# Performance work log

Hardware: AMD Instinct MI355X
Metric: run time of the kernel (lower is better)

## Reference

```python
import jax, jax.numpy as jnp
import numpy as np

MARGIN = 1.0

def setup_inputs() -> dict:
    key = jax.random.key(0)
    k1, k2 = jax.random.split(key)
    B, D, NUM_CLASSES = 4096, 512, 64
    inputs = jax.random.normal(k1, (B, D), dtype=jnp.float32)
    labels = jax.random.randint(k2, (B,), 0, NUM_CLASSES, dtype=jnp.int64)
    return {"inputs": inputs, "labels": labels}

def reference(inputs, labels):
    # Full pairwise squared L2 distances via the ||a-b||^2 = ||a||^2 + ||b||^2 - 2 a.b expansion
    sq = jnp.sum(inputs * inputs, axis=1)                      # [B]
    d2 = sq[:, None] + sq[None, :] - 2.0 * (inputs @ inputs.T)  # [B, B]
    d2 = jnp.maximum(d2, 0.0)
    # Safe sqrt: zero (self) distances get exactly 0 without NaN-producing sqrt(0) grads
    nz = d2 > 1e-12
    dist = jnp.where(nz, jnp.sqrt(jnp.where(nz, d2, 1.0)), 0.0)  # [B, B]

    mask = labels[:, None] == labels[None, :]                   # [B, B] same-class mask (includes self)
    mask_f = mask.astype(dist.dtype)

    # Per-anchor: mean distance to positives (self included, contributing 0, as in the torch loop)
    ap_mean = jnp.sum(dist * mask_f, axis=1) / jnp.sum(mask_f, axis=1)  # [B]
    # Per-anchor: min distance to negatives
    an_min = jnp.min(jnp.where(mask, jnp.inf, dist), axis=1)            # [B]

    tmp = ap_mean - an_min + MARGIN                             # [B]
    # `if tmp > 0: loss += tmp` over the batch == sum of relu(tmp)
    return jnp.sum(jnp.maximum(tmp, 0.0))
```

## Files before the change

kernel.cpp:

```cpp
#include <hip/hip_runtime.h>
#include <hip/hip_bf16.h>

typedef unsigned short u16;
typedef unsigned int u32;
typedef __attribute__((ext_vector_type(8))) short short8;
typedef __attribute__((ext_vector_type(8))) u16 ushort8;
typedef __attribute__((ext_vector_type(4))) float f32x4;

#define B_SZ 4096
#define D_SZ 512
#define NCLS 64
#define NT   32
#define NBLK (NT * (NT + 1) / 2)


__device__ __forceinline__ u16 f2bf(float x) {
    union { float f; u32 u; } a; a.f = x;
    u32 r = a.u + 0x7fffu + ((a.u >> 16) & 1u);
    return (u16)(r >> 16);
}

__device__ __forceinline__ void gload16(const void* g, void* l) {
    __builtin_amdgcn_global_load_lds(
        (const __attribute__((address_space(1))) u32*)g,
        (__attribute__((address_space(3))) u32*)l,
        16, 0, 0);
}


__global__ __launch_bounds__(256) void prep_kernel(
    const float* __restrict__ in, u16* __restrict__ bfout,
    float* __restrict__ sq, float* __restrict__ ap_sum, u32* __restrict__ an_min)
{
    const int wave = threadIdx.x >> 6, l = threadIdx.x & 63;
    const int row = blockIdx.x * 4 + wave;
    const float* p = in + (size_t)row * D_SZ + l * 8;
    float4 v0 = *(const float4*)p;
    float4 v1 = *(const float4*)(p + 4);
    float s = v0.x*v0.x + v0.y*v0.y + v0.z*v0.z + v0.w*v0.w
            + v1.x*v1.x + v1.y*v1.y + v1.z*v1.z + v1.w*v1.w;
    ushort8 o;
    o[0]=f2bf(v0.x); o[1]=f2bf(v0.y); o[2]=f2bf(v0.z); o[3]=f2bf(v0.w);
    o[4]=f2bf(v1.x); o[5]=f2bf(v1.y); o[6]=f2bf(v1.z); o[7]=f2bf(v1.w);
    *(ushort8*)(bfout + (size_t)row * D_SZ + l * 8) = o;
    #pragma unroll
    for (int off = 1; off < 64; off <<= 1) s += __shfl_xor(s, off);
    if (l == 0) {
        sq[row] = s;
        ap_sum[row] = 0.0f;
        an_min[row] = 0x7f800000u;
    }
}


__global__ __launch_bounds__(256) void tile_kernel(
    const u16* __restrict__ bfin, const int* __restrict__ lab,
    const float* __restrict__ sq, float* __restrict__ ap_sum, u32* __restrict__ an_min)
{
    __shared__ u16 As[128 * 32];
    __shared__ u16 Bs[128 * 32];
    __shared__ float sqA[128], sqB[128];
    __shared__ int labA[128], labB[128];

    const int t = threadIdx.x;

    const int bid = blockIdx.x;
    int tm = (int)((__builtin_sqrtf(8.0f * (float)bid + 1.0f) - 1.0f) * 0.5f);
    while ((tm + 1) * (tm + 2) / 2 <= bid) ++tm;
    while (tm * (tm + 1) / 2 > bid) --tm;
    const int tn = bid - tm * (tm + 1) / 2;
    const bool diag = (tm == tn);

    const int rowBase = tm * 128;
    const int colBase = tn * 128;

    if (t < 128) { labA[t] = lab[rowBase + t]; sqA[t] = sq[rowBase + t]; }
    else { int u = t - 128; labB[u] = lab[colBase + u]; sqB[u] = sq[colBase + u]; }

    const int wave = t >> 6, lane = t & 63;
    const int wr = wave >> 1, wc = wave & 1;
    const int g = lane >> 4, c = lane & 15;

    f32x4 acc[4][4];
    #pragma unroll
    for (int i = 0; i < 4; ++i)
        #pragma unroll
        for (int j = 0; j < 4; ++j)
            acc[i][j] = (f32x4){0.f, 0.f, 0.f, 0.f};

    const u16* gA = bfin + (size_t)(rowBase + (t >> 2)) * D_SZ + (t & 3) * 8;
    const u16* gB = bfin + (size_t)(colBase + (t >> 2)) * D_SZ + (t & 3) * 8;

    #pragma unroll 1
    for (int kk = 0; kk < D_SZ / 32; ++kk) {
        gload16(gA + kk * 32,             As + t * 8);
        gload16(gA + kk * 32 + 64 * D_SZ, As + 2048 + t * 8);
        gload16(gB + kk * 32,             Bs + t * 8);
        gload16(gB + kk * 32 + 64 * D_SZ, Bs + 2048 + t * 8);
        __syncthreads();

        short8 a[4], b[4];
        #pragma unroll
        for (int mi = 0; mi < 4; ++mi)
            a[mi] = *(const short8*)&As[(wr * 64 + mi * 16 + c) * 32 + g * 8];
        #pragma unroll
        for (int ni = 0; ni < 4; ++ni)
            b[ni] = *(const short8*)&Bs[(wc * 64 + ni * 16 + c) * 32 + g * 8];

        #pragma unroll
        for (int mi = 0; mi < 4; ++mi)
            #pragma unroll
            for (int ni = 0; ni < 4; ++ni)
                acc[mi][ni] = __builtin_amdgcn_mfma_f32_16x16x32_bf16(a[mi], b[ni], acc[mi][ni], 0, 0, 0);
        __syncthreads();
    }

    float sc[4], mc[4];
    #pragma unroll
    for (int ni = 0; ni < 4; ++ni) { sc[ni] = 0.0f; mc[ni] = __builtin_inff(); }

    #pragma unroll
    for (int mi = 0; mi < 4; ++mi) {
        #pragma unroll
        for (int r = 0; r < 4; ++r) {
            const int lrow = wr * 64 + mi * 16 + g * 4 + r;
            const int i = rowBase + lrow;
            const int li = labA[lrow];
            const float sqi = sqA[lrow];
            float s = 0.0f;
            float mn = __builtin_inff();
            #pragma unroll
            for (int ni = 0; ni < 4; ++ni) {
                const int lcol = wc * 64 + ni * 16 + c;
                float d2 = sqi + sqB[lcol] - 2.0f * acc[mi][ni][r];
                d2 = fmaxf(d2, 0.0f);
                float dist = (d2 > 1e-12f) ? __builtin_sqrtf(d2) : 0.0f;
                if (diag && lrow == lcol) dist = 0.0f;
                if (li == labB[lcol]) { s += dist; sc[ni] += dist; }
                else                  { mn = fminf(mn, dist); mc[ni] = fminf(mc[ni], dist); }
            }
            #pragma unroll
            for (int off = 1; off < 16; off <<= 1) {
                s += __shfl_xor(s, off);
                mn = fminf(mn, __shfl_xor(mn, off));
            }
            if (c == 0) {
                atomicAdd(&ap_sum[i], s);
                atomicMin(&an_min[i], __float_as_uint(mn));
            }
        }
    }

    if (!diag) {
        #pragma unroll
        for (int ni = 0; ni < 4; ++ni) {
            float s = sc[ni], mn = mc[ni];
            s += __shfl_xor(s, 16); s += __shfl_xor(s, 32);
            mn = fminf(mn, __shfl_xor(mn, 16)); mn = fminf(mn, __shfl_xor(mn, 32));
            if (lane < 16) {
                const int j = colBase + wc * 64 + ni * 16 + c;
                atomicAdd(&ap_sum[j], s);
                atomicMin(&an_min[j], __float_as_uint(mn));
            }
        }
    }
}


__global__ __launch_bounds__(1024) void final_kernel(
    const float* __restrict__ ap_sum, const u32* __restrict__ an_min,
    const int* __restrict__ lab, float* __restrict__ out)
{
    __shared__ int cnt[NCLS];
    __shared__ float wsum[16];
    const int t = threadIdx.x;
    if (t < NCLS) cnt[t] = 0;
    __syncthreads();
    for (int i = t; i < B_SZ; i += 1024) atomicAdd(&cnt[lab[i]], 1);
    __syncthreads();
    float v = 0.0f;
    for (int i = t; i < B_SZ; i += 1024) {
        float apm = ap_sum[i] / (float)cnt[lab[i]];
        float anm = __uint_as_float(an_min[i]);
        v += fmaxf(apm - anm + 1.0f, 0.0f);
    }
    #pragma unroll
    for (int off = 1; off < 64; off <<= 1) v += __shfl_xor(v, off);
    if ((t & 63) == 0) wsum[t >> 6] = v;
    __syncthreads();
    if (t == 0) {
        float s = 0.0f;
        #pragma unroll
        for (int w = 0; w < 16; ++w) s += wsum[w];
        out[0] = s;
    }
}


extern "C" void kernel_launch(void* const* d_in, const int* in_sizes, int n_in,
                              void* d_out, int out_size, void* d_ws, size_t ws_size,
                              hipStream_t stream) {
    const float* inputs = (const float*)d_in[0];
    const int* labels = (const int*)d_in[1];
    float* out = (float*)d_out;

    char* ws = (char*)d_ws;
    float* ap_sum = (float*)ws;
    u32* an_min = (u32*)(ws + 16384);
    float* sq = (float*)(ws + 32768);
    u16* bfin = (u16*)(ws + 65536);

    prep_kernel<<<dim3(B_SZ / 4), dim3(256), 0, stream>>>(inputs, bfin, sq, ap_sum, an_min);
    tile_kernel<<<dim3(NBLK), dim3(256), 0, stream>>>(bfin, labels, sq, ap_sum, an_min);
    final_kernel<<<dim3(1), dim3(1024), 0, stream>>>(ap_sum, an_min, labels, out);
}
```

Baseline: 43.65 us.

## Double-buffer LDS tiles with XOR swizzle and skip duplicate B load on diagonal

The GEMM K-loop now double-buffers the A/B LDS tiles, prefetching the next K-slice while MFMAs run on the current one, and removes one of the two barriers per iteration. LDS rows are XOR-swizzled by row index to cut bank conflicts on the short8 fragment reads. Diagonal tiles load only A and reuse it as B, which saves global traffic. This doubles LDS use per block, which may reduce occupancy.

```diff
diff --git a/kernel.cpp b/kernel.cpp
--- a/kernel.cpp
+++ b/kernel.cpp
@@ -10,8 +10,11 @@
 #define B_SZ 4096
 #define D_SZ 512
 #define NCLS 64
+#define BK   32
+#define NKK  (D_SZ / BK)
 #define NT   32
 #define NBLK (NT * (NT + 1) / 2)
+#define TILE_ELEMS (128 * BK)
 
 
 __device__ __forceinline__ u16 f2bf(float x) {
@@ -25,6 +28,16 @@
         (const __attribute__((address_space(1))) u32*)g,
         (__attribute__((address_space(3))) u32*)l,
         16, 0, 0);
+}
+
+__device__ __forceinline__ void stage_tile32(const u16* __restrict__ gsrc, u16* dst, int t) {
+    #pragma unroll
+    for (int q = 0; q < 2; ++q) {
+        const int s = t + q * 256;
+        const int r = s >> 2;
+        const int col = ((s & 3) ^ (r & 3)) << 3;
+        gload16(gsrc + (size_t)r * D_SZ + col, dst + s * 8);
+    }
 }
 
 
@@ -57,8 +70,8 @@
     const u16* __restrict__ bfin, const int* __restrict__ lab,
     const float* __restrict__ sq, float* __restrict__ ap_sum, u32* __restrict__ an_min)
 {
-    __shared__ u16 As[128 * 32];
-    __shared__ u16 Bs[128 * 32];
+    __shared__ u16 As[2][TILE_ELEMS];
+    __shared__ u16 Bs[2][TILE_ELEMS];
     __shared__ float sqA[128], sqB[128];
     __shared__ int labA[128], labB[128];
 
@@ -88,30 +101,39 @@
         for (int j = 0; j < 4; ++j)
             acc[i][j] = (f32x4){0.f, 0.f, 0.f, 0.f};
 
-    const u16* gA = bfin + (size_t)(rowBase + (t >> 2)) * D_SZ + (t & 3) * 8;
-    const u16* gB = bfin + (size_t)(colBase + (t >> 2)) * D_SZ + (t & 3) * 8;
+    const u16* gA = bfin + (size_t)rowBase * D_SZ;
+    const u16* gB = bfin + (size_t)colBase * D_SZ;
+
+    stage_tile32(gA, As[0], t);
+    if (!diag) stage_tile32(gB, Bs[0], t);
+    __syncthreads();
+
+    const int sw = (g ^ (c & 3)) << 3;
 
     #pragma unroll 1
-    for (int kk = 0; kk < D_SZ / 32; ++kk) {
-        gload16(gA + kk * 32,             As + t * 8);
-        gload16(gA + kk * 32 + 64 * D_SZ, As + 2048 + t * 8);
-        gload16(gB + kk * 32,             Bs + t * 8);
-        gload16(gB + kk * 32 + 64 * D_SZ, Bs + 2048 + t * 8);
-        __syncthreads();
+    for (int kk = 0; kk < NKK; ++kk) {
+        const int cur = kk & 1;
+        if (kk + 1 < NKK) {
+            stage_tile32(gA + (kk + 1) * BK, As[cur ^ 1], t);
+            if (!diag) stage_tile32(gB + (kk + 1) * BK, Bs[cur ^ 1], t);
+        }
+        const u16* abuf = As[cur];
+        const u16* bbuf = diag ? abuf : Bs[cur];
 
         short8 a[4], b[4];
         #pragma unroll
         for (int mi = 0; mi < 4; ++mi)
-            a[mi] = *(const short8*)&As[(wr * 64 + mi * 16 + c) * 32 + g * 8];
+            a[mi] = *(const short8*)&abuf[(wr * 64 + mi * 16 + c) * BK + sw];
         #pragma unroll
         for (int ni = 0; ni < 4; ++ni)
-            b[ni] = *(const short8*)&Bs[(wc * 64 + ni * 16 + c) * 32 + g * 8];
+            b[ni] = *(const short8*)&bbuf[(wc * 64 + ni * 16 + c) * BK + sw];
 
         #pragma unroll
         for (int mi = 0; mi < 4; ++mi)
             #pragma unroll
             for (int ni = 0; ni < 4; ++ni)
                 acc[mi][ni] = __builtin_amdgcn_mfma_f32_16x16x32_bf16(a[mi], b[ni], acc[mi][ni], 0, 0, 0);
+
         __syncthreads();
     }
 
```

Result: faster. 41.00 us (-6.1%).
